# Optimization experiments

Hardware: AMD Instinct MI355X
Metric: run time of the kernel (lower is better)

The kernel has to match this reference:

```python
import jax, jax.numpy as jnp
import numpy as np

N = 30000      # nodes
E = 240000     # edges (before self-loops)
D = 128        # vec_dim
L = 6          # GAT layers
NEG_SLOPE = 0.2
EPS = 1e-5


def setup_inputs() -> dict:
    key = jax.random.key(0)
    ks = jax.random.split(key, 20)
    s = 1.0 / np.sqrt(D)
    inp = {
        "x": jax.random.randint(ks[0], (N,), 0, 120),
        "edge_index": jax.random.randint(ks[1], (2, E), 0, N),
        "emb": jax.random.normal(ks[2], (120, D), jnp.float32) * 0.05,
        # stacked GATv2Conv params for 6 layers (heads=1)
        "Wl": jax.random.normal(ks[3], (L, D, D), jnp.float32) * s,
        "bl": jnp.zeros((L, D), jnp.float32),
        "Wr": jax.random.normal(ks[4], (L, D, D), jnp.float32) * s,
        "br": jnp.zeros((L, D), jnp.float32),
        "att": jax.random.normal(ks[5], (L, D), jnp.float32) * s,
        "conv_bias": jnp.zeros((L, D), jnp.float32),
        # PyG LayerNorm (applied after layers 0..4)
        "ln_g": jnp.ones((L - 1, D), jnp.float32),
        "ln_b": jnp.zeros((L - 1, D), jnp.float32),
        # outer Linear + BatchNorm1d
        "lin_W": jax.random.normal(ks[6], (D, D), jnp.float32) * s,
        "lin_b": jnp.zeros((D,), jnp.float32),
        "bn_g": jnp.ones((D,), jnp.float32),
        "bn_b": jnp.zeros((D,), jnp.float32),
    }
    return inp


def _segment_softmax(score, seg, num_segments):
    # numerically stable softmax over variable-degree neighborhoods
    m = jax.ops.segment_max(score, seg, num_segments=num_segments)
    ex = jnp.exp(score - m[seg])
    denom = jax.ops.segment_sum(ex, seg, num_segments=num_segments)
    return ex / denom[seg]


def _gat_forward(h, src, dst, Wl, bl, Wr, br, att, conv_bias, ln_g, ln_b):
    xg = h
    for i in range(L):
        xl = xg @ Wl[i] + bl[i]          # [N, D] source transform
        xr = xg @ Wr[i] + br[i]          # [N, D] target transform
        # GATv2 attention: a^T LeakyReLU(x_l[j] + x_r[i]) per edge j->i
        e = jax.nn.leaky_relu(xl[src] + xr[dst], NEG_SLOPE)   # [E2, D]
        score = e @ att[i]                                     # [E2]
        alpha = _segment_softmax(score, dst, N)                # [E2]
        msg = alpha[:, None] * xl[src]                         # [E2, D]
        xg = jax.ops.segment_sum(msg, dst, num_segments=N) + conv_bias[i]
        if i < L - 1:
            # PyG LayerNorm(mode='graph'): global mean/std, per-channel affine
            mu = xg.mean()
            var = ((xg - mu) ** 2).mean()
            xg = (xg - mu) / jnp.sqrt(var + EPS) * ln_g[i] + ln_b[i]
            xg = jax.nn.relu(xg)
            # dropout(0.1) is identity in eval mode
    return xg


def reference(x, edge_index, emb, Wl, bl, Wr, br, att, conv_bias,
              ln_g, ln_b, lin_W, lin_b, bn_g, bn_b):
    h = emb[x]                                      # [N, D]
    # PyG GATv2Conv default add_self_loops=True
    loops = jnp.arange(N, dtype=edge_index.dtype)
    src = jnp.concatenate([edge_index[0], loops])   # [E2]
    dst = jnp.concatenate([edge_index[1], loops])   # [E2]
    xg = _gat_forward(h, src, dst, Wl, bl, Wr, br, att, conv_bias, ln_g, ln_b)
    out = (h + xg) @ lin_W + lin_b                  # [N, D]
    # BatchNorm1d (batch-statistics / train-mode math)
    mu = out.mean(axis=0)
    var = out.var(axis=0)
    out = (out - mu) / jnp.sqrt(var + EPS) * bn_g + bn_b
    return out
```

## Files before the change

### kernel.cpp

```cpp
#include <hip/hip_runtime.h>
#include <math.h>

#define N_NODES 30000
#define N_EDGES 240000
#define E2 (N_EDGES + N_NODES)
#define D 128
#define LAYERS 6
#define NEG_SLOPE 0.2f
#define LN_EPS 1e-5f

typedef unsigned short u16;
typedef unsigned int u32;
using bfrag = __attribute__((ext_vector_type(8))) short;
using f32x4 = __attribute__((ext_vector_type(4))) float;

__device__ inline u16 f2bf(float f) {
    u32 u = __float_as_uint(f);
    u32 r = u + 0x7fffu + ((u >> 16) & 1u);
    return (u16)(r >> 16);
}
__device__ inline u32 pack2(float a, float b) { return (u32)f2bf(a) | ((u32)f2bf(b) << 16); }
__device__ inline float bflo(u32 u) { return __uint_as_float(u << 16); }
__device__ inline float bfhi(u32 u) { return __uint_as_float(u & 0xffff0000u); }
__device__ inline u32 bfadd2(u32 a, u32 b) {
    return pack2(bflo(a) + bflo(b), bfhi(a) + bfhi(b));
}

__global__ __launch_bounds__(256) void wt_convert(const float* __restrict__ Wl,
        const float* __restrict__ Wr, const float* __restrict__ linW, u16* __restrict__ wt)
{
    __shared__ u16 tile[128 * 129];
    int b = blockIdx.x;
    const float* src = (b == 12) ? linW
                     : ((b & 1) ? Wr + (size_t)(b >> 1) * 16384 : Wl + (size_t)(b >> 1) * 16384);
    int t = threadIdx.x;
    #pragma unroll 4
    for (int i = 0; i < 64; i++) {
        int idx = t + 256 * i;
        int k = idx >> 7, n = idx & 127;
        tile[n * 129 + k] = f2bf(src[idx]);
    }
    __syncthreads();
    u16* dst = wt + (size_t)b * 16384;
    #pragma unroll 4
    for (int i = 0; i < 64; i++) {
        int idx = t + 256 * i;
        int n = idx >> 7, k = idx & 127;
        dst[idx] = tile[n * 129 + k];
    }
}

__global__ __launch_bounds__(256) void embed_kernel(const int* __restrict__ x,
        const float* __restrict__ emb, u16* __restrict__ h_bf)
{
    int idx = blockIdx.x * 256 + threadIdx.x;
    if (idx >= N_NODES * 32) return;
    int n = idx >> 5, q = idx & 31;
    float4 v = ((const float4*)(emb + (size_t)x[n] * D))[q];
    ushort4 o;
    o.x = f2bf(v.x); o.y = f2bf(v.y); o.z = f2bf(v.z); o.w = f2bf(v.w);
    ((ushort4*)h_bf)[idx] = o;
}

__global__ __launch_bounds__(256) void hist_kernel(const int* __restrict__ ei, int* __restrict__ cnt)
{
    int e = blockIdx.x * 256 + threadIdx.x;
    if (e >= E2) return;
    int d = (e < N_EDGES) ? ei[N_EDGES + e] : (e - N_EDGES);
    atomicAdd(&cnt[d], 1);
}

__global__ __launch_bounds__(1024) void scan1_kernel(const int* __restrict__ cnt,
        int* __restrict__ lscan, int* __restrict__ bsum)
{
    __shared__ int wtot[16];
    int t = threadIdx.x, lane = t & 63, w = t >> 6;
    int i = blockIdx.x * 1024 + t;
    int v = (i < N_NODES) ? cnt[i] : 0;
    int s = v;
    #pragma unroll
    for (int off = 1; off < 64; off <<= 1) {
        int u = __shfl_up(s, off);
        if (lane >= off) s += u;
    }
    if (lane == 63) wtot[w] = s;
    __syncthreads();
    if (t < 16) {
        int xv = wtot[t];
        #pragma unroll
        for (int off = 1; off < 16; off <<= 1) {
            int u = __shfl_up(xv, off);
            if (t >= off) xv += u;
        }
        wtot[t] = xv;
    }
    __syncthreads();
    int incl = ((w == 0) ? 0 : wtot[w - 1]) + s;
    if (i < N_NODES) lscan[i] = incl;
    if (t == 0) bsum[blockIdx.x] = wtot[15];
}

__global__ __launch_bounds__(1024) void scan3_kernel(const int* __restrict__ lscan,
        const int* __restrict__ bsum, const int* __restrict__ cnt,
        int* __restrict__ row_off, int* __restrict__ cursor)
{
    __shared__ int sboff;
    if (threadIdx.x < 64) {
        int v = (threadIdx.x < 30) ? bsum[threadIdx.x] : 0;
        int s = v;
        #pragma unroll
        for (int off = 1; off < 64; off <<= 1) {
            int u = __shfl_up(s, off);
            if ((int)threadIdx.x >= off) s += u;
        }
        if (threadIdx.x == blockIdx.x) sboff = s - v;
    }
    __syncthreads();
    int i = blockIdx.x * 1024 + threadIdx.x;
    if (i == 0) row_off[0] = 0;
    if (i < N_NODES) {
        int r = lscan[i] + sboff;
        row_off[i + 1] = r;
        cursor[i] = r - cnt[i];
    }
}

__global__ __launch_bounds__(256) void scatter_kernel(const int* __restrict__ ei,
        int* __restrict__ cursor, int* __restrict__ csr_src)
{
    int e = blockIdx.x * 256 + threadIdx.x;
    if (e >= E2) return;
    int s, d;
    if (e < N_EDGES) { s = ei[e]; d = ei[N_EDGES + e]; }
    else             { s = e - N_EDGES; d = s; }
    int pos = atomicAdd(&cursor[d], 1);
    csr_src[pos] = s;
}

template<bool LN, bool DUAL, bool OUTF>
__global__ __launch_bounds__(256) void gemm_mfma(
    const u16* __restrict__ Abf, const u16* __restrict__ A2bf,
    const float* __restrict__ Aln, const float* __restrict__ lnacc,
    const float* __restrict__ lng, const float* __restrict__ lnb,
    const u16* __restrict__ Wt1, const float* __restrict__ b1,
    float* __restrict__ C1f, u16* __restrict__ C1h,
    const u16* __restrict__ Wt2, const float* __restrict__ b2, u16* __restrict__ C2h,
    int M)
{
    __shared__ u16 As[32 * 136];
    __shared__ float sLN[2];
    int t = threadIdx.x;
    int m0 = blockIdx.x * 32;
    int lane = t & 63, w = t >> 6;
    int n16 = lane & 15, quad = lane >> 4;
    int c0 = w * 32;

    bfrag bW1[2][4], bW2[2][4];
    #pragma unroll
    for (int c = 0; c < 2; c++)
        #pragma unroll
        for (int ks = 0; ks < 4; ks++)
            bW1[c][ks] = *(const bfrag*)(Wt1 + (size_t)(c0 + c * 16 + n16) * 128 + ks * 32 + quad * 8);
    if (DUAL) {
        #pragma unroll
        for (int c = 0; c < 2; c++)
            #pragma unroll
            for (int ks = 0; ks < 4; ks++)
                bW2[c][ks] = *(const bfrag*)(Wt2 + (size_t)(c0 + c * 16 + n16) * 128 + ks * 32 + quad * 8);
    }

    if (LN) {
        if (w == 0) {
            float2 v = ((const float2*)lnacc)[lane];
            float s = v.x, ss = v.y;
            #pragma unroll
            for (int off = 32; off > 0; off >>= 1) {
                s += __shfl_xor(s, off); ss += __shfl_xor(ss, off);
            }
            if (lane == 0) {
                const float invM = 1.f / ((float)N_NODES * (float)D);
                float mu  = s * invM;
                float var = ss * invM - mu * mu;
                sLN[0] = mu;
                sLN[1] = rsqrtf(var + LN_EPS);
            }
        }
        __syncthreads();
        float mu = sLN[0], inv = sLN[1];
        #pragma unroll
        for (int i = 0; i < 4; i++) {
            int idx = t + 256 * i;
            int row = idx >> 5, c4 = idx & 31;
            int gr = m0 + row;
            float4 v = make_float4(0.f, 0.f, 0.f, 0.f);
            if (gr < M) v = ((const float4*)(Aln + (size_t)gr * D))[c4];
            float4 gv = ((const float4*)lng)[c4];
            float4 bv = ((const float4*)lnb)[c4];
            v.x = (v.x - mu) * inv * gv.x + bv.x; v.x = v.x > 0.f ? v.x : 0.f;
            v.y = (v.y - mu) * inv * gv.y + bv.y; v.y = v.y > 0.f ? v.y : 0.f;
            v.z = (v.z - mu) * inv * gv.z + bv.z; v.z = v.z > 0.f ? v.z : 0.f;
            v.w = (v.w - mu) * inv * gv.w + bv.w; v.w = v.w > 0.f ? v.w : 0.f;
            uint2 pk = make_uint2(pack2(v.x, v.y), pack2(v.z, v.w));
            *(uint2*)&As[row * 136 + c4 * 4] = pk;
        }
    } else {
        #pragma unroll
        for (int i = 0; i < 2; i++) {
            int idx = t + 256 * i;
            int row = idx >> 4, c16 = idx & 15;
            int gr = m0 + row;
            uint4 v = make_uint4(0u, 0u, 0u, 0u);
            if (gr < M) {
                v = ((const uint4*)(Abf + (size_t)gr * 128))[c16];
                if (A2bf) {
                    uint4 u = ((const uint4*)(A2bf + (size_t)gr * 128))[c16];
                    v.x = bfadd2(v.x, u.x); v.y = bfadd2(v.y, u.y);
                    v.z = bfadd2(v.z, u.z); v.w = bfadd2(v.w, u.w);
                }
            }
            *(uint4*)&As[row * 136 + c16 * 8] = v;
        }
    }
    __syncthreads();

    f32x4 zero = {0.f, 0.f, 0.f, 0.f};
    f32x4 acc1[2][2] = {{zero, zero}, {zero, zero}};
    f32x4 acc2[2][2] = {{zero, zero}, {zero, zero}};
    #pragma unroll
    for (int ks = 0; ks < 4; ks++) {
        bfrag a[2];
        #pragma unroll
        for (int r = 0; r < 2; r++)
            a[r] = *(const bfrag*)&As[(r * 16 + n16) * 136 + ks * 32 + quad * 8];
        #pragma unroll
        for (int r = 0; r < 2; r++)
            #pragma unroll
            for (int c = 0; c < 2; c++) {
                acc1[r][c] = __builtin_amdgcn_mfma_f32_16x16x32_bf16(a[r], bW1[c][ks], acc1[r][c], 0, 0, 0);
                if (DUAL)
                    acc2[r][c] = __builtin_amdgcn_mfma_f32_16x16x32_bf16(a[r], bW2[c][ks], acc2[r][c], 0, 0, 0);
            }
    }

    float bv1[2] = { b1[c0 + n16], b1[c0 + 16 + n16] };
    #pragma unroll
    for (int r = 0; r < 2; r++)
        #pragma unroll
        for (int c = 0; c < 2; c++)
            #pragma unroll
            for (int reg = 0; reg < 4; reg++) {
                int grow = m0 + r * 16 + quad * 4 + reg;
                if (grow < M) {
                    float val = acc1[r][c][reg] + bv1[c];
                    int col = c0 + c * 16 + n16;
                    if (OUTF) C1f[(size_t)grow * 128 + col] = val;
                    else      C1h[(size_t)grow * 128 + col] = f2bf(val);
                }
            }
    if (DUAL) {
        float bv2[2] = { b2[c0 + n16], b2[c0 + 16 + n16] };
        #pragma unroll
        for (int r = 0; r < 2; r++)
            #pragma unroll
            for (int c = 0; c < 2; c++)
                #pragma unroll
                for (int reg = 0; reg < 4; reg++) {
                    int grow = m0 + r * 16 + quad * 4 + reg;
                    if (grow < M)
                        C2h[(size_t)grow * 128 + c0 + c * 16 + n16] = f2bf(acc2[r][c][reg] + bv2[c]);
                }
    }
}

__global__ __launch_bounds__(256) void gat_agg(
    const u16* __restrict__ xl, const u16* __restrict__ xr,
    const int* __restrict__ row_off, const int* __restrict__ csr_src,
    const float* __restrict__ att, const float* __restrict__ conv_bias,
    float* __restrict__ xg, u16* __restrict__ xg_bf, float* __restrict__ lnacc)
{
    int wave = threadIdx.x >> 6, lane = threadIdx.x & 63;
    int node = blockIdx.x * 4 + wave;
    int g = lane >> 4, q = lane & 15;

    uint4 rr = *(const uint4*)(xr + (size_t)node * 128 + q * 8);
    float4 r0 = make_float4(bflo(rr.x), bfhi(rr.x), bflo(rr.y), bfhi(rr.y));
    float4 r1 = make_float4(bflo(rr.z), bfhi(rr.z), bflo(rr.w), bfhi(rr.w));
    float4 av0 = ((const float4*)att)[2 * q];
    float4 av1 = ((const float4*)att)[2 * q + 1];

    int s0 = row_off[node], s1 = row_off[node + 1];
    float denom = 0.f;
    float4 a0 = make_float4(0.f, 0.f, 0.f, 0.f), a1 = a0;

    #pragma unroll 2
    for (int s = s0 + g; s < s1; s += 4) {
        int src = csr_src[s];
        uint4 raw = *(const uint4*)(xl + (size_t)src * 128 + q * 8);
        float4 v0 = make_float4(bflo(raw.x), bfhi(raw.x), bflo(raw.y), bfhi(raw.y));
        float4 v1 = make_float4(bflo(raw.z), bfhi(raw.z), bflo(raw.w), bfhi(raw.w));
        float pr = 0.f, tt;
        tt = v0.x + r0.x; tt = tt > 0.f ? tt : NEG_SLOPE * tt; pr += av0.x * tt;
        tt = v0.y + r0.y; tt = tt > 0.f ? tt : NEG_SLOPE * tt; pr += av0.y * tt;
        tt = v0.z + r0.z; tt = tt > 0.f ? tt : NEG_SLOPE * tt; pr += av0.z * tt;
        tt = v0.w + r0.w; tt = tt > 0.f ? tt : NEG_SLOPE * tt; pr += av0.w * tt;
        tt = v1.x + r1.x; tt = tt > 0.f ? tt : NEG_SLOPE * tt; pr += av1.x * tt;
        tt = v1.y + r1.y; tt = tt > 0.f ? tt : NEG_SLOPE * tt; pr += av1.y * tt;
        tt = v1.z + r1.z; tt = tt > 0.f ? tt : NEG_SLOPE * tt; pr += av1.z * tt;
        tt = v1.w + r1.w; tt = tt > 0.f ? tt : NEG_SLOPE * tt; pr += av1.w * tt;
        #pragma unroll
        for (int off = 1; off < 16; off <<= 1) pr += __shfl_xor(pr, off);
        float wv = __expf(pr);
        denom += wv;
        a0.x += wv * v0.x; a0.y += wv * v0.y; a0.z += wv * v0.z; a0.w += wv * v0.w;
        a1.x += wv * v1.x; a1.y += wv * v1.y; a1.z += wv * v1.z; a1.w += wv * v1.w;
    }

    #pragma unroll
    for (int msk = 16; msk <= 32; msk <<= 1) {
        denom += __shfl_xor(denom, msk);
        a0.x += __shfl_xor(a0.x, msk); a0.y += __shfl_xor(a0.y, msk);
        a0.z += __shfl_xor(a0.z, msk); a0.w += __shfl_xor(a0.w, msk);
        a1.x += __shfl_xor(a1.x, msk); a1.y += __shfl_xor(a1.y, msk);
        a1.z += __shfl_xor(a1.z, msk); a1.w += __shfl_xor(a1.w, msk);
    }

    float4 cb0 = ((const float4*)conv_bias)[2 * q];
    float4 cb1 = ((const float4*)conv_bias)[2 * q + 1];
    float inv = 1.f / denom;
    float4 o0, o1;
    o0.x = a0.x * inv + cb0.x; o0.y = a0.y * inv + cb0.y;
    o0.z = a0.z * inv + cb0.z; o0.w = a0.w * inv + cb0.w;
    o1.x = a1.x * inv + cb1.x; o1.y = a1.y * inv + cb1.y;
    o1.z = a1.z * inv + cb1.z; o1.w = a1.w * inv + cb1.w;

    if (xg_bf) {
        if (g == 0) {
            uint4 pk = make_uint4(pack2(o0.x, o0.y), pack2(o0.z, o0.w),
                                  pack2(o1.x, o1.y), pack2(o1.z, o1.w));
            ((uint4*)(xg_bf + (size_t)node * 128))[q] = pk;
        }
    } else {
        if (g == 0) {
            ((float4*)(xg + (size_t)node * 128))[2 * q]     = o0;
            ((float4*)(xg + (size_t)node * 128))[2 * q + 1] = o1;
        }
        float s  = o0.x + o0.y + o0.z + o0.w + o1.x + o1.y + o1.z + o1.w;
        float ss = o0.x*o0.x + o0.y*o0.y + o0.z*o0.z + o0.w*o0.w
                 + o1.x*o1.x + o1.y*o1.y + o1.z*o1.z + o1.w*o1.w;
        #pragma unroll
        for (int off = 1; off < 16; off <<= 1) { s += __shfl_xor(s, off); ss += __shfl_xor(ss, off); }
        __shared__ float sred[8];
        if (lane == 0) { sred[wave] = s; sred[4 + wave] = ss; }
        __syncthreads();
        if (threadIdx.x == 0) {
            int slot = blockIdx.x & 63;
            atomicAdd(&lnacc[2 * slot],     sred[0] + sred[1] + sred[2] + sred[3]);
            atomicAdd(&lnacc[2 * slot + 1], sred[4] + sred[5] + sred[6] + sred[7]);
        }
    }
}

__global__ __launch_bounds__(256) void bn_reduce(const float* __restrict__ out, float* __restrict__ acc)
{
    int c = threadIdx.x & 127;
    int rg = threadIdx.x >> 7;
    float s = 0.f, ss = 0.f;
    for (int r = blockIdx.x * 2 + rg; r < N_NODES; r += gridDim.x * 2) {
        float v = out[(size_t)r * D + c];
        s += v; ss += v * v;
    }
    __shared__ float ls[256], lss[256];
    ls[threadIdx.x] = s; lss[threadIdx.x] = ss;
    __syncthreads();
    if (rg == 0) {
        s  = ls[c]  + ls[c + 128];
        ss = lss[c] + lss[c + 128];
        atomicAdd(&acc[c], s);
        atomicAdd(&acc[128 + c], ss);
    }
}

__global__ __launch_bounds__(256) void bn_apply(float* __restrict__ out, const float* __restrict__ acc,
        const float* __restrict__ g, const float* __restrict__ b)
{
    int idx = blockIdx.x * 256 + threadIdx.x;
    if (idx >= N_NODES * 32) return;
    int c4 = idx & 31;
    const float invN = 1.f / (float)N_NODES;
    float4 s1 = ((const float4*)(acc))[c4];
    float4 s2 = ((const float4*)(acc + 128))[c4];
    float4 gv = ((const float4*)g)[c4];
    float4 bv = ((const float4*)b)[c4];
    float4 v = ((float4*)out)[idx];
    float mu, var, inv;
    mu = s1.x * invN; var = s2.x * invN - mu * mu; inv = rsqrtf(var + LN_EPS);
    v.x = (v.x - mu) * inv * gv.x + bv.x;
    mu = s1.y * invN; var = s2.y * invN - mu * mu; inv = rsqrtf(var + LN_EPS);
    v.y = (v.y - mu) * inv * gv.y + bv.y;
    mu = s1.z * invN; var = s2.z * invN - mu * mu; inv = rsqrtf(var + LN_EPS);
    v.z = (v.z - mu) * inv * gv.z + bv.z;
    mu = s1.w * invN; var = s2.w * invN - mu * mu; inv = rsqrtf(var + LN_EPS);
    v.w = (v.w - mu) * inv * gv.w + bv.w;
    ((float4*)out)[idx] = v;
}

extern "C" void kernel_launch(void* const* d_in, const int* in_sizes, int n_in,
                              void* d_out, int out_size, void* d_ws, size_t ws_size,
                              hipStream_t stream)
{
    const int*   x    = (const int*)d_in[0];
    const int*   ei   = (const int*)d_in[1];
    const float* emb  = (const float*)d_in[2];
    const float* Wl   = (const float*)d_in[3];
    const float* bl   = (const float*)d_in[4];
    const float* Wr   = (const float*)d_in[5];
    const float* br   = (const float*)d_in[6];
    const float* att  = (const float*)d_in[7];
    const float* cbias= (const float*)d_in[8];
    const float* lng  = (const float*)d_in[9];
    const float* lnb  = (const float*)d_in[10];
    const float* linW = (const float*)d_in[11];
    const float* linb = (const float*)d_in[12];
    const float* bng  = (const float*)d_in[13];
    const float* bnb  = (const float*)d_in[14];
    float* out = (float*)d_out;

    char* p = (char*)d_ws;
    float* xg    = (float*)p; p += (size_t)N_NODES * D * 4;
    u16*   xl_bf = (u16*)p;   p += (size_t)N_NODES * D * 2;
    u16*   xr_bf = (u16*)p;   p += (size_t)N_NODES * D * 2;
    u16*   xg_bf = (u16*)p;   p += (size_t)N_NODES * D * 2;
    u16*   h_bf  = (u16*)p;   p += (size_t)N_NODES * D * 2;
    u16*   wt    = (u16*)p;   p += (size_t)13 * 16384 * 2;
    int* cnt     = (int*)p; p += ((N_NODES * 4 + 255) / 256) * 256;
    int* lscan   = (int*)p; p += ((N_NODES * 4 + 255) / 256) * 256;
    int* row_off = (int*)p; p += (((N_NODES + 1) * 4 + 255) / 256) * 256;
    int* cursor  = (int*)p; p += ((N_NODES * 4 + 255) / 256) * 256;
    int* csr_src = (int*)p; p += ((E2 * 4 + 255) / 256) * 256;
    int* bsum    = (int*)p; p += 256;
    float* accs  = (float*)p; p += 4096;

    hipMemsetAsync(cnt, 0, N_NODES * 4, stream);
    hipMemsetAsync(accs, 0, 4096, stream);

    wt_convert<<<13, 256, 0, stream>>>(Wl, Wr, linW, wt);
    embed_kernel<<<3750, 256, 0, stream>>>(x, emb, h_bf);
    hist_kernel<<<(E2 + 255) / 256, 256, 0, stream>>>(ei, cnt);
    scan1_kernel<<<30, 1024, 0, stream>>>(cnt, lscan, bsum);
    scan3_kernel<<<30, 1024, 0, stream>>>(lscan, bsum, cnt, row_off, cursor);
    scatter_kernel<<<(E2 + 255) / 256, 256, 0, stream>>>(ei, cursor, csr_src);

    for (int i = 0; i < LAYERS; i++) {
        if (i == 0) {
            gemm_mfma<false, true, false><<<938, 256, 0, stream>>>(
                h_bf, nullptr, nullptr, nullptr, nullptr, nullptr,
                wt + (size_t)0 * 16384, bl + 0, nullptr, xl_bf,
                wt + (size_t)1 * 16384, br + 0, xr_bf, N_NODES);
        } else {
            gemm_mfma<true, true, false><<<938, 256, 0, stream>>>(
                nullptr, nullptr, xg, accs + (i - 1) * 128,
                lng + (size_t)(i - 1) * D, lnb + (size_t)(i - 1) * D,
                wt + (size_t)(2 * i) * 16384, bl + i * D, nullptr, xl_bf,
                wt + (size_t)(2 * i + 1) * 16384, br + i * D, xr_bf, N_NODES);
        }
        gat_agg<<<7500, 256, 0, stream>>>(xl_bf, xr_bf, row_off, csr_src,
            att + i * D, cbias + i * D, xg,
            (i == LAYERS - 1) ? xg_bf : nullptr,
            (i < LAYERS - 1) ? (accs + i * 128) : nullptr);
    }
    gemm_mfma<false, false, true><<<938, 256, 0, stream>>>(
        xg_bf, h_bf, nullptr, nullptr, nullptr, nullptr,
        wt + (size_t)12 * 16384, linb, out, nullptr,
        nullptr, nullptr, nullptr, N_NODES);
    bn_reduce<<<256, 256, 0, stream>>>(out, accs + 640);
    bn_apply<<<3750, 256, 0, stream>>>(out, accs + 640, bng, bnb);
}
```

Before: 582.3 us.

## Fuse embedding and BN stats into GEMMs; widen per-edge lanes in GAT aggregation

Folds the embedding gather into the first dual GEMM and the BatchNorm column sum/sumsq into the final GEMM epilogue, using 16 striped atomic slots. This removes the embed_kernel and bn_reduce launches along with their extra passes over memory. The GAT aggregation now uses 8 lanes per edge, each covering 16 channels, so each wave processes 8 edges at once, and it reduces across lanes with DPP instead of shuffles. In exchange, registers per lane go up and bn_apply has to sum the 16 slots on every thread.

Result: no change. 581.0 us (-0.2%).

```diff
diff --git a/kernel.cpp b/kernel.cpp
--- a/kernel.cpp
+++ b/kernel.cpp
@@ -24,6 +24,13 @@
 __device__ inline float bfhi(u32 u) { return __uint_as_float(u & 0xffff0000u); }
 __device__ inline u32 bfadd2(u32 a, u32 b) {
     return pack2(bflo(a) + bflo(b), bfhi(a) + bfhi(b));
+}
+
+__device__ inline float red8_dpp(float x) {
+    x += __int_as_float(__builtin_amdgcn_update_dpp(0, __float_as_int(x), 0xB1, 0xF, 0xF, true));
+    x += __int_as_float(__builtin_amdgcn_update_dpp(0, __float_as_int(x), 0x4E, 0xF, 0xF, true));
+    x += __int_as_float(__builtin_amdgcn_update_dpp(0, __float_as_int(x), 0x141, 0xF, 0xF, true));
+    return x;
 }
 
 __global__ __launch_bounds__(256) void wt_convert(const float* __restrict__ Wl,
@@ -50,18 +57,6 @@
     }
 }
 
-__global__ __launch_bounds__(256) void embed_kernel(const int* __restrict__ x,
-        const float* __restrict__ emb, u16* __restrict__ h_bf)
-{
-    int idx = blockIdx.x * 256 + threadIdx.x;
-    if (idx >= N_NODES * 32) return;
-    int n = idx >> 5, q = idx & 31;
-    float4 v = ((const float4*)(emb + (size_t)x[n] * D))[q];
-    ushort4 o;
-    o.x = f2bf(v.x); o.y = f2bf(v.y); o.z = f2bf(v.z); o.w = f2bf(v.w);
-    ((ushort4*)h_bf)[idx] = o;
-}
-
 __global__ __launch_bounds__(256) void hist_kernel(const int* __restrict__ ei, int* __restrict__ cnt)
 {
     int e = blockIdx.x * 256 + threadIdx.x;
@@ -137,15 +132,16 @@
     csr_src[pos] = s;
 }
 
-template<bool LN, bool DUAL, bool OUTF>
+template<bool LN, bool DUAL, bool OUTF, bool EMB>
 __global__ __launch_bounds__(256) void gemm_mfma(
     const u16* __restrict__ Abf, const u16* __restrict__ A2bf,
     const float* __restrict__ Aln, const float* __restrict__ lnacc,
     const float* __restrict__ lng, const float* __restrict__ lnb,
+    const int* __restrict__ xidx, const float* __restrict__ emb, u16* __restrict__ h_out,
     const u16* __restrict__ Wt1, const float* __restrict__ b1,
     float* __restrict__ C1f, u16* __restrict__ C1h,
     const u16* __restrict__ Wt2, const float* __restrict__ b2, u16* __restrict__ C2h,
-    int M)
+    float* __restrict__ bnacc, int M)
 {
     __shared__ u16 As[32 * 136];
     __shared__ float sLN[2];
@@ -203,6 +199,23 @@
             uint2 pk = make_uint2(pack2(v.x, v.y), pack2(v.z, v.w));
             *(uint2*)&As[row * 136 + c4 * 4] = pk;
         }
+    } else if (EMB) {
+        #pragma unroll
+        for (int i = 0; i < 2; i++) {
+            int idx = t + 256 * i;
+            int row = idx >> 4, c16 = idx & 15;
+            int gr = m0 + row;
+            uint4 v = make_uint4(0u, 0u, 0u, 0u);
+            if (gr < M) {
+                const float* er = emb + (size_t)xidx[gr] * D + c16 * 8;
+                float4 e0 = ((const float4*)er)[0];
+                float4 e1 = ((const float4*)er)[1];
+                v.x = pack2(e0.x, e0.y); v.y = pack2(e0.z, e0.w);
+                v.z = pack2(e1.x, e1.y); v.w = pack2(e1.z, e1.w);
+                ((uint4*)(h_out + (size_t)gr * 128))[c16] = v;
+            }
+            *(uint4*)&As[row * 136 + c16 * 8] = v;
+        }
     } else {
         #pragma unroll
         for (int i = 0; i < 2; i++) {
@@ -243,6 +256,7 @@
     }
 
     float bv1[2] = { b1[c0 + n16], b1[c0 + 16 + n16] };
+    float bns[2] = {0.f, 0.f}, bnss[2] = {0.f, 0.f};
     #pragma unroll
     for (int r = 0; r < 2; r++)
         #pragma unroll
@@ -253,10 +267,33 @@
                 if (grow < M) {
                     float val = acc1[r][c][reg] + bv1[c];
                     int col = c0 + c * 16 + n16;
-                    if (OUTF) C1f[(size_t)grow * 128 + col] = val;
-                    else      C1h[(size_t)grow * 128 + col] = f2bf(val);
+                    if (OUTF) {
+                        C1f[(size_t)grow * 128 + col] = val;
+                        bns[c] += val; bnss[c] += val * val;
+                    } else {
+                        C1h[(size_t)grow * 128 + col] = f2bf(val);
+                    }
                 }
             }
+    if (OUTF) {
+        #pragma unroll
+        for (int c = 0; c < 2; c++) {
+            #pragma unroll
+            for (int msk = 16; msk <= 32; msk <<= 1) {
+                bns[c]  += __shfl_xor(bns[c], msk);
+                bnss[c] += __shfl_xor(bnss[c], msk);
+            }
+        }
+        if (quad == 0) {
+            float* base = bnacc + (size_t)(blockIdx.x & 15) * 256;
+            #pragma unroll
+            for (int c = 0; c < 2; c++) {
+                int col = c0 + c * 16 + n16;
+                atomicAdd(&base[col], bns[c]);
+                atomicAdd(&base[128 + col], bnss[c]);
+            }
+        }
+    }
     if (DUAL) {
         float bv2[2] = { b2[c0 + n16], b2[c0 + 16 + n16] };
         #pragma unroll
@@ -280,24 +317,32 @@
 {
     int wave = threadIdx.x >> 6, lane = threadIdx.x & 63;
     int node = blockIdx.x * 4 + wave;
-    int g = lane >> 4, q = lane & 15;
-
-    uint4 rr = *(const uint4*)(xr + (size_t)node * 128 + q * 8);
-    float4 r0 = make_float4(bflo(rr.x), bfhi(rr.x), bflo(rr.y), bfhi(rr.y));
-    float4 r1 = make_float4(bflo(rr.z), bfhi(rr.z), bflo(rr.w), bfhi(rr.w));
-    float4 av0 = ((const float4*)att)[2 * q];
-    float4 av1 = ((const float4*)att)[2 * q + 1];
+    int g = lane >> 3, q = lane & 7;
+
+    const uint4* xrow = (const uint4*)(xr + (size_t)node * 128);
+    uint4 rrA = xrow[2 * q], rrB = xrow[2 * q + 1];
+    float4 r0 = make_float4(bflo(rrA.x), bfhi(rrA.x), bflo(rrA.y), bfhi(rrA.y));
+    float4 r1 = make_float4(bflo(rrA.z), bfhi(rrA.z), bflo(rrA.w), bfhi(rrA.w));
+    float4 r2 = make_float4(bflo(rrB.x), bfhi(rrB.x), bflo(rrB.y), bfhi(rrB.y));
+    float4 r3 = make_float4(bflo(rrB.z), bfhi(rrB.z), bflo(rrB.w), bfhi(rrB.w));
+    float4 av0 = ((const float4*)att)[4 * q];
+    float4 av1 = ((const float4*)att)[4 * q + 1];
+    float4 av2 = ((const float4*)att)[4 * q + 2];
+    float4 av3 = ((const float4*)att)[4 * q + 3];
 
     int s0 = row_off[node], s1 = row_off[node + 1];
     float denom = 0.f;
-    float4 a0 = make_float4(0.f, 0.f, 0.f, 0.f), a1 = a0;
+    float4 a0 = make_float4(0.f, 0.f, 0.f, 0.f), a1 = a0, a2 = a0, a3 = a0;
 
     #pragma unroll 2
-    for (int s = s0 + g; s < s1; s += 4) {
+    for (int s = s0 + g; s < s1; s += 8) {
         int src = csr_src[s];
-        uint4 raw = *(const uint4*)(xl + (size_t)src * 128 + q * 8);
-        float4 v0 = make_float4(bflo(raw.x), bfhi(raw.x), bflo(raw.y), bfhi(raw.y));
-        float4 v1 = make_float4(bflo(raw.z), bfhi(raw.z), bflo(raw.w), bfhi(raw.w));
+        const uint4* row = (const uint4*)(xl + (size_t)src * 128);
+        uint4 rawA = row[2 * q], rawB = row[2 * q + 1];
+        float4 v0 = make_float4(bflo(rawA.x), bfhi(rawA.x), bflo(rawA.y), bfhi(rawA.y));
+        float4 v1 = make_float4(bflo(rawA.z), bfhi(rawA.z), bflo(rawA.w), bfhi(rawA.w));
+        float4 v2 = make_float4(bflo(rawB.x), bfhi(rawB.x), bflo(rawB.y), bfhi(rawB.y));
+        float4 v3 = make_float4(bflo(rawB.z), bfhi(rawB.z), bflo(rawB.w), bfhi(rawB.w));
         float pr = 0.f, tt;
         tt = v0.x + r0.x; tt = tt > 0.f ? tt : NEG_SLOPE * tt; pr += av0.x * tt;
         tt = v0.y + r0.y; tt = tt > 0.f ? tt : NEG_SLOPE * tt; pr += av0.y * tt;
@@ -307,48 +352,73 @@
         tt = v1.y + r1.y; tt = tt > 0.f ? tt : NEG_SLOPE * tt; pr += av1.y * tt;
         tt = v1.z + r1.z; tt = tt > 0.f ? tt : NEG_SLOPE * tt; pr += av1.z * tt;
         tt = v1.w + r1.w; tt = tt > 0.f ? tt : NEG_SLOPE * tt; pr += av1.w * tt;
-        #pragma unroll
-        for (int off = 1; off < 16; off <<= 1) pr += __shfl_xor(pr, off);
+        tt = v2.x + r2.x; tt = tt > 0.f ? tt : NEG_SLOPE * tt; pr += av2.x * tt;
+        tt = v2.y + r2.y; tt = tt > 0.f ? tt : NEG_SLOPE * tt; pr += av2.y * tt;
+        tt = v2.z + r2.z; tt = tt > 0.f ? tt : NEG_SLOPE * tt; pr += av2.z * tt;
+        tt = v2.w + r2.w; tt = tt > 0.f ? tt : NEG_SLOPE * tt; pr += av2.w * tt;
+        tt = v3.x + r3.x; tt = tt > 0.f ? tt : NEG_SLOPE * tt; pr += av3.x * tt;
+        tt = v3.y + r3.y; tt = tt > 0.f ? tt : NEG_SLOPE * tt; pr += av3.y * tt;
+        tt = v3.z + r3.z; tt = tt > 0.f ? tt : NEG_SLOPE * tt; pr += av3.z * tt;
+        tt = v3.w + r3.w; tt = tt > 0.f ? tt : NEG_SLOPE * tt; pr += av3.w * tt;
+        pr = red8_dpp(pr);
         float wv = __expf(pr);
         denom += wv;
         a0.x += wv * v0.x; a0.y += wv * v0.y; a0.z += wv * v0.z; a0.w += wv * v0.w;
         a1.x += wv * v1.x; a1.y += wv * v1.y; a1.z += wv * v1.z; a1.w += wv * v1.w;
+        a2.x += wv * v2.x; a2.y += wv * v2.y; a2.z += wv * v2.z; a2.w += wv * v2.w;
+        a3.x += wv * v3.x; a3.y += wv * v3.y; a3.z += wv * v3.z; a3.w += wv * v3.w;
     }
 
     #pragma unroll
-    for (int msk = 16; msk <= 32; msk <<= 1) {
+    for (int msk = 8; msk <= 32; msk <<= 1) {
         denom += __shfl_xor(denom, msk);
         a0.x += __shfl_xor(a0.x, msk); a0.y += __shfl_xor(a0.y, msk);
         a0.z += __shfl_xor(a0.z, msk); a0.w += __shfl_xor(a0.w, msk);
         a1.x += __shfl_xor(a1.x, msk); a1.y += __shfl_xor(a1.y, msk);
         a1.z += __shfl_xor(a1.z, msk); a1.w += __shfl_xor(a1.w, msk);
-    }
-
-    float4 cb0 = ((const float4*)conv_bias)[2 * q];
-    float4 cb1 = ((const float4*)conv_bias)[2 * q + 1];
+        a2.x += __shfl_xor(a2.x, msk); a2.y += __shfl_xor(a2.y, msk);
+        a2.z += __shfl_xor(a2.z, msk); a2.w += __shfl_xor(a2.w, msk);
+        a3.x += __shfl_xor(a3.x, msk); a3.y += __shfl_xor(a3.y, msk);
+        a3.z += __shfl_xor(a3.z, msk); a3.w += __shfl_xor(a3.w, msk);
+    }
+
+    float4 cb0 = ((const float4*)conv_bias)[4 * q];
+    float4 cb1 = ((const float4*)conv_bias)[4 * q + 1];
+    float4 cb2 = ((const float4*)conv_bias)[4 * q + 2];
+    float4 cb3 = ((const float4*)conv_bias)[4 * q + 3];
     float inv = 1.f / denom;
-    float4 o0, o1;
+    float4 o0, o1, o2, o3;
     o0.x = a0.x * inv + cb0.x; o0.y = a0.y * inv + cb0.y;
     o0.z = a0.z * inv + cb0.z; o0.w = a0.w * inv + cb0.w;
     o1.x = a1.x * inv + cb1.x; o1.y = a1.y * inv + cb1.y;
     o1.z = a1.z * inv + cb1.z; o1.w = a1.w * inv + cb1.w;
+    o2.x = a2.x * inv + cb2.x; o2.y = a2.y * inv + cb2.y;
+    o2.z = a2.z * inv + cb2.z; o2.w = a2.w * inv + cb2.w;
+    o3.x = a3.x * inv + cb3.x; o3.y = a3.y * inv + cb3.y;
+    o3.z = a3.z * inv + cb3.z; o3.w = a3.w * inv + cb3.w;
 
     if (xg_bf) {
         if (g == 0) {
-            uint4 pk = make_uint4(pack2(o0.x, o0.y), pack2(o0.z, o0.w),
-                                  pack2(o1.x, o1.y), pack2(o1.z, o1.w));
-            ((uint4*)(xg_bf + (size_t)node * 128))[q] = pk;
+            uint4 pk0 = make_uint4(pack2(o0.x, o0.y), pack2(o0.z, o0.w),
+                                   pack2(o1.x, o1.y), pack2(o1.z, o1.w));
+            uint4 pk1 = make_uint4(pack2(o2.x, o2.y), pack2(o2.z, o2.w),
+                                   pack2(o3.x, o3.y), pack2(o3.z, o3.w));
+            ((uint4*)(xg_bf + (size_t)node * 128))[2 * q]     = pk0;
+            ((uint4*)(xg_bf + (size_t)node * 128))[2 * q + 1] = pk1;
         }
     } else {
         if (g == 0) {
-            ((float4*)(xg + (size_t)node * 128))[2 * q]     = o0;
-            ((float4*)(xg + (size_t)node * 128))[2 * q + 1] = o1;
-        }
-        float s  = o0.x + o0.y + o0.z + o0.w + o1.x + o1.y + o1.z + o1.w;
+            float4* od = (float4*)(xg + (size_t)node * 128);
+            od[4 * q] = o0; od[4 * q + 1] = o1; od[4 * q + 2] = o2; od[4 * q + 3] = o3;
+        }
+        float s  = o0.x + o0.y + o0.z + o0.w + o1.x + o1.y + o1.z + o1.w
+                 + o2.x + o2.y + o2.z + o2.w + o3.x + o3.y + o3.z + o3.w;
         float ss = o0.x*o0.x + o0.y*o0.y + o0.z*o0.z + o0.w*o0.w
-                 + o1.x*o1.x + o1.y*o1.y + o1.z*o1.z + o1.w*o1.w;
-        #pragma unroll
-        for (int off = 1; off < 16; off <<= 1) { s += __shfl_xor(s, off); ss += __shfl_xor(ss, off); }
+                 + o1.x*o1.x + o1.y*o1.y + o1.z*o1.z + o1.w*o1.w
+                 + o2.x*o2.x + o2.y*o2.y + o2.z*o2.z + o2.w*o2.w
+                 + o3.x*o3.x + o3.y*o3.y + o3.z*o3.z + o3.w*o3.w;
+        s  = red8_dpp(s);
+        ss = red8_dpp(ss);
         __shared__ float sred[8];
         if (lane == 0) { sred[wave] = s; sred[4 + wave] = ss; }
         __syncthreads();
@@ -360,38 +430,24 @@
     }
 }
 
-__global__ __launch_bounds__(256) void bn_reduce(const float* __restrict__ out, float* __restrict__ acc)
-{
-    int c = threadIdx.x & 127;
-    int rg = threadIdx.x >> 7;
-    float s = 0.f, ss = 0.f;
-    for (int r = blockIdx.x * 2 + rg; r < N_NODES; r += gridDim.x * 2) {
-        float v = out[(size_t)r * D + c];
-        s += v; ss += v * v;
-    }
-    __shared__ float ls[256], lss[256];
-    ls[threadIdx.x] = s; lss[threadIdx.x] = ss;
-    __syncthreads();
-    if (rg == 0) {
-        s  = ls[c]  + ls[c + 128];
-        ss = lss[c] + lss[c + 128];
-        atomicAdd(&acc[c], s);
-        atomicAdd(&acc[128 + c], ss);
-    }
-}
-
 __global__ __launch_bounds__(256) void bn_apply(float* __restrict__ out, const float* __restrict__ acc,
         const float* __restrict__ g, const float* __restrict__ b)
 {
     int idx = blockIdx.x * 256 + threadIdx.x;
     if (idx >= N_NODES * 32) return;
     int c4 = idx & 31;
-    const float invN = 1.f / (float)N_NODES;
-    float4 s1 = ((const float4*)(acc))[c4];
-    float4 s2 = ((const float4*)(acc + 128))[c4];
+    float4 s1 = make_float4(0.f, 0.f, 0.f, 0.f), s2 = s1;
+    #pragma unroll
+    for (int slot = 0; slot < 16; slot++) {
+        float4 a = ((const float4*)(acc + slot * 256))[c4];
+        float4 d = ((const float4*)(acc + slot * 256 + 128))[c4];
+        s1.x += a.x; s1.y += a.y; s1.z += a.z; s1.w += a.w;
+        s2.x += d.x; s2.y += d.y; s2.z += d.z; s2.w += d.w;
+    }
     float4 gv = ((const float4*)g)[c4];
     float4 bv = ((const float4*)b)[c4];
     float4 v = ((float4*)out)[idx];
+    const float invN = 1.f / (float)N_NODES;
     float mu, var, inv;
     mu = s1.x * invN; var = s2.x * invN - mu * mu; inv = rsqrtf(var + LN_EPS);
     v.x = (v.x - mu) * inv * gv.x + bv.x;
@@ -438,13 +494,12 @@
     int* cursor  = (int*)p; p += ((N_NODES * 4 + 255) / 256) * 256;
     int* csr_src = (int*)p; p += ((E2 * 4 + 255) / 256) * 256;
     int* bsum    = (int*)p; p += 256;
-    float* accs  = (float*)p; p += 4096;
+    float* accs  = (float*)p; p += 20480;
 
     hipMemsetAsync(cnt, 0, N_NODES * 4, stream);
-    hipMemsetAsync(accs, 0, 4096, stream);
+    hipMemsetAsync(accs, 0, (640 + 4096) * 4, stream);
 
     wt_convert<<<13, 256, 0, stream>>>(Wl, Wr, linW, wt);
-    embed_kernel<<<3750, 256, 0, stream>>>(x, emb, h_bf);
     hist_kernel<<<(E2 + 255) / 256, 256, 0, stream>>>(ei, cnt);
     scan1_kernel<<<30, 1024, 0, stream>>>(cnt, lscan, bsum);
     scan3_kernel<<<30, 1024, 0, stream>>>(lscan, bsum, cnt, row_off, cursor);
@@ -452,26 +507,28 @@
 
     for (int i = 0; i < LAYERS; i++) {
         if (i == 0) {
-            gemm_mfma<false, true, false><<<938, 256, 0, stream>>>(
-                h_bf, nullptr, nullptr, nullptr, nullptr, nullptr,
+            gemm_mfma<false, true, false, true><<<938, 256, 0, stream>>>(
+                nullptr, nullptr, nullptr, nullptr, nullptr, nullptr,
+                x, emb, h_bf,
                 wt + (size_t)0 * 16384, bl + 0, nullptr, xl_bf,
-                wt + (size_t)1 * 16384, br + 0, xr_bf, N_NODES);
+                wt + (size_t)1 * 16384, br + 0, xr_bf, nullptr, N_NODES);
         } else {
-            gemm_mfma<true, true, false><<<938, 256, 0, stream>>>(
+            gemm_mfma<true, true, false, false><<<938, 256, 0, stream>>>(
                 nullptr, nullptr, xg, accs + (i - 1) * 128,
                 lng + (size_t)(i - 1) * D, lnb + (size_t)(i - 1) * D,
+                nullptr, nullptr, nullptr,
                 wt + (size_t)(2 * i) * 16384, bl + i * D, nullptr, xl_bf,
-                wt + (size_t)(2 * i + 1) * 16384, br + i * D, xr_bf, N_NODES);
+                wt + (size_t)(2 * i + 1) * 16384, br + i * D, xr_bf, nullptr, N_NODES);
         }
         gat_agg<<<7500, 256, 0, stream>>>(xl_bf, xr_bf, row_off, csr_src,
             att + i * D, cbias + i * D, xg,
             (i == LAYERS - 1) ? xg_bf : nullptr,
             (i < LAYERS - 1) ? (accs + i * 128) : nullptr);
     }
-    gemm_mfma<false, false, true><<<938, 256, 0, stream>>>(
+    gemm_mfma<false, false, true, false><<<938, 256, 0, stream>>>(
         xg_bf, h_bf, nullptr, nullptr, nullptr, nullptr,
+        nullptr, nullptr, nullptr,
         wt + (size_t)12 * 16384, linb, out, nullptr,
-        nullptr, nullptr, nullptr, N_NODES);
-    bn_reduce<<<256, 256, 0, stream>>>(out, accs + 640);
+        nullptr, nullptr, nullptr, accs + 640, N_NODES);
     bn_apply<<<3750, 256, 0, stream>>>(out, accs + 640, bng, bnb);
 }
```
